# Performance work log

Measured on AMD Instinct MI355X. Metric: run time of the kernel, lower is better.

## Reference

```python
import jax, jax.numpy as jnp
import numpy as np

B, C, H, L = 8, 1, 512, 4096


def setup_inputs() -> dict:
    key = jax.random.key(0)
    k1, k2, k3, k4, k5 = jax.random.split(key, 5)
    u = jax.random.normal(k1, (B, H, L), dtype=jnp.float32)
    # SSM kernel k (C, H, L): stand-in for HippoSSKernel output, scaled so the
    # length-L convolution has O(1) variance.
    k = jax.random.normal(k2, (C, H, L), dtype=jnp.float32) * (1.0 / np.sqrt(L))
    D = jax.random.normal(k3, (C, H), dtype=jnp.float32)
    # output_linear: pointwise linear (C*H) -> H
    W = jax.random.normal(k4, (H, C * H), dtype=jnp.float32) * (1.0 / np.sqrt(C * H))
    b = jax.random.normal(k5, (H,), dtype=jnp.float32) * 0.01
    return {"u": u, "k": k, "D": D, "W": W, "b": b}


def reference(u, k, D, W, b):
    # u: (B, H, L), k: (C, H, L), D: (C, H), W: (H, C*H), b: (H,)
    Lq = u.shape[-1]
    n = 2 * Lq  # zero-padded FFT length for linear (non-circular) convolution
    k_f = jnp.fft.rfft(k, n=n)                       # (C, H, n//2+1) complex
    u_f = jnp.fft.rfft(u, n=n)                       # (B, H, n//2+1) complex
    y_f = jnp.einsum('bhl,chl->bchl', u_f, k_f)      # freq-domain multiply
    y = jnp.fft.irfft(y_f, n=n)[..., :Lq]            # (B, C, H, L)
    y = y + jnp.einsum('bhl,ch->bchl', u, D)         # skip term
    Bq, Cq, Hq, _ = y.shape
    y = y.reshape(Bq, Cq * Hq, Lq)                   # (B, C*H, L)
    y = jax.nn.gelu(y, approximate=False)            # torch GELU (erf)
    y = jnp.einsum('bcl,dc->bdl', y, W) + b[None, :, None]  # pointwise linear
    return y
```

## Files before the change

### kernel.cpp

```cpp
#include <hip/hip_runtime.h>
#include <hip/hip_bf16.h>
#include <math.h>

#define L_DIM 4096
#define H_DIM 512
#define B_DIM 8
#define SEG 2048

typedef __attribute__((ext_vector_type(8))) short short8;
typedef __attribute__((ext_vector_type(4))) float floatx4;

__device__ __forceinline__ unsigned f2bf(float f) {
    unsigned x = __float_as_uint(f);
    return (x + 0x7fffu + ((x >> 16) & 1u)) >> 16;
}

__global__ __launch_bounds__(256, 3) void conv_gelu_mfma(
    const float* __restrict__ u,
    const float* __restrict__ kk,
    const float* __restrict__ Dp,
    unsigned short* __restrict__ g,
    const float* __restrict__ W,
    unsigned short* __restrict__ Wb)
{
    __shared__ __align__(16) unsigned short kA[4144];
    __shared__ __align__(16) unsigned short kB[4144];
    __shared__ __align__(16) unsigned short us[8][2104];

    const int h   = blockIdx.x;
    const int Lb  = blockIdx.y << 10;
    const int tid = threadIdx.x;
    const int lane = tid & 63;
    const int w   = tid >> 6;
    const int i   = lane & 15;
    const int q   = lane >> 4;
    const int b   = i & 7;
    const int s   = i >> 3;

    if (Wb != nullptr && blockIdx.y == 0) {
        const float* wsrc = W + (size_t)h * H_DIM;
        unsigned short* wdst = Wb + (size_t)h * H_DIM;
        wdst[tid]       = (unsigned short)f2bf(wsrc[tid]);
        wdst[tid + 256] = (unsigned short)f2bf(wsrc[tid + 256]);
    }

    const float* kh = kk + (size_t)h * L_DIM;

    for (int p = tid; p < 4144; p += 256) {
        int t1 = L_DIM + 15 - p;
        int t2 = L_DIM + 14 - p;
        float v1 = (t1 >= 0 && t1 < L_DIM) ? kh[t1] : 0.0f;
        float v2 = (t2 >= 0 && t2 < L_DIM) ? kh[t2] : 0.0f;
        kA[p] = (unsigned short)f2bf(v1);
        kB[p] = (unsigned short)f2bf(v2);
    }

    floatx4 acc[8];
    #pragma unroll
    for (int t = 0; t < 8; t++) acc[t] = (floatx4){0.f, 0.f, 0.f, 0.f};

    const char* kbase = (const char*)((i & 1) ? kA : kB);
    const int aconst = 2 * (L_DIM + ((i & 1) ? 15 : 14) - i + 8 * q);
    const int basew = Lb + 32 * w;

    union AFrag { int x[4]; short8 v; };

    for (int seg = 0; seg < 2; seg++) {
        const int ms = seg * SEG;
        const int mstart = (seg == 0) ? -32 : SEG;
        const int segmax = ms + SEG - 32;
        if (seg == 1) {
            if (Lb + 992 < SEG) break;
            __syncthreads();
        }
        for (int e = tid * 4; e < 2096; e += 1024) {
            int m = ms - 32 + e;
            #pragma unroll
            for (int bb = 0; bb < 8; bb++) {
                float4 v = make_float4(0.f, 0.f, 0.f, 0.f);
                if (m >= 0 && m < L_DIM)
                    v = *(const float4*)(u + ((size_t)bb * H_DIM + h) * L_DIM + m);
                unsigned lo = f2bf(v.x) | (f2bf(v.y) << 16);
                unsigned hi = f2bf(v.z) | (f2bf(v.w) << 16);
                *(uint2*)&us[bb][e] = make_uint2(lo, hi);
            }
        }
        __syncthreads();

        const char* bbase = (const char*)&us[b][0] + 2 * (32 - ms + 16 * s + 8 * q);
        const char* ab = kbase + aconst;

        for (int c = 0; c < 4; c++) {
            const int c32 = 32 * c;
            const int rel = basew - c32;
            const int j_hi = (rel - mstart) >> 7;
            int j_lo = (rel - segmax + 127) >> 7;
            if (j_lo < -7) j_lo = -7;
            if (j_hi < j_lo) continue;
            const int n = j_hi - j_lo + 1;
            int n_pos = 0;
            if (j_hi >= 0) n_pos = j_hi - ((j_lo > 0) ? j_lo : 0) + 1;
            const int n_main = n_pos & ~7;

            const char* abase = ab - 2 * c32;
            const char* bb0 = bbase + 2 * (rel - 128 * j_hi);

            for (int jb = 0; jb < n_main; jb += 8) {
                const int j_g = j_hi - jb;
                const char* aptr = abase - 256 * (j_g + 7);
                const char* bptr = bb0 + 256 * jb;

                AFrag As[15];
                short8 Bs[8];
                Bs[0] = *(const short8*)(bptr);
                #pragma unroll
                for (int d = 7; d < 15; d++) {
                    const int* ap = (const int*)(aptr + 256 * (14 - d));
                    As[d].x[0] = ap[0]; As[d].x[1] = ap[1];
                    As[d].x[2] = ap[2]; As[d].x[3] = ap[3];
                }
                #pragma unroll
                for (int k = 1; k < 8; k++) {
                    Bs[k] = *(const short8*)(bptr + 256 * k);
                    const int* ap = (const int*)(aptr + 256 * (14 - (7 - k)));
                    As[7 - k].x[0] = ap[0]; As[7 - k].x[1] = ap[1];
                    As[7 - k].x[2] = ap[2]; As[7 - k].x[3] = ap[3];
                }
                __builtin_amdgcn_sched_barrier(0);

                #pragma unroll
                for (int k = 0; k < 8; k++)
                    #pragma unroll
                    for (int t = 0; t < 8; t++)
                        acc[t] = __builtin_amdgcn_mfma_f32_16x16x32_bf16(
                            As[7 - k + t].v, Bs[k], acc[t], 0, 0, 0);
            }

            if (n_main < n) {
                const int j_top = j_hi - n_main;
                AFrag Wd[8];
                #pragma unroll
                for (int d = 1; d < 8; d++) {
                    const int dd = c32 + (j_top + d) * 128;
                    if (dd >= 0) {
                        const int* ap = (const int*)(ab - 2 * dd);
                        Wd[d].x[0] = ap[0]; Wd[d].x[1] = ap[1];
                        Wd[d].x[2] = ap[2]; Wd[d].x[3] = ap[3];
                    } else {
                        Wd[d].x[0] = 0; Wd[d].x[1] = 0; Wd[d].x[2] = 0; Wd[d].x[3] = 0;
                    }
                }
                for (int jb = n_main; jb < n; jb += 8) {
                    #pragma unroll
                    for (int k = 0; k < 8; k++) {
                        const int jj = jb + k;
                        if (jj < n) {
                            const int dd0 = c32 + (j_hi - jj) * 128;
                            AFrag nf;
                            if (dd0 >= 0) {
                                const int* ap = (const int*)(ab - 2 * dd0);
                                nf.x[0] = ap[0]; nf.x[1] = ap[1];
                                nf.x[2] = ap[2]; nf.x[3] = ap[3];
                            } else {
                                nf.x[0] = 0; nf.x[1] = 0; nf.x[2] = 0; nf.x[3] = 0;
                            }
                            Wd[(8 - k) & 7] = nf;
                            short8 bf = *(const short8*)(bb0 + 256 * jj);
                            #pragma unroll
                            for (int t = 0; t < 8; t++)
                                acc[t] = __builtin_amdgcn_mfma_f32_16x16x32_bf16(
                                    Wd[(t - k) & 7].v, bf, acc[t], 0, 0, 0);
                        }
                    }
                }
            }
        }
    }

    const float Dh = Dp[h];
    #pragma unroll
    for (int t = 0; t < 8; t++) {
        const int l0 = Lb + 32 * w + 128 * t;
        const int lb2 = l0 + 16 * s + 4 * q;
        const size_t off = ((size_t)b * H_DIM + h) * L_DIM + lb2;
        float4 uv = *(const float4*)(u + off);
        float y0 = acc[t][0] + uv.x * Dh;
        float y1 = acc[t][1] + uv.y * Dh;
        float y2 = acc[t][2] + uv.z * Dh;
        float y3 = acc[t][3] + uv.w * Dh;
        const float c = 0.70710678118654752f;
        float g0 = 0.5f * y0 * (1.0f + erff(y0 * c));
        float g1 = 0.5f * y1 * (1.0f + erff(y1 * c));
        float g2 = 0.5f * y2 * (1.0f + erff(y2 * c));
        float g3 = 0.5f * y3 * (1.0f + erff(y3 * c));
        unsigned lo = f2bf(g0) | (f2bf(g1) << 16);
        unsigned hi = f2bf(g2) | (f2bf(g3) << 16);
        *(uint2*)(g + off) = make_uint2(lo, hi);
    }
}

template <bool PREW>
__global__ __launch_bounds__(256, 2) void pointwise_mfma(
    const unsigned short* __restrict__ g,
    const unsigned short* __restrict__ Wb,
    const float* __restrict__ W,
    const float* __restrict__ bias,
    float* __restrict__ out)
{
    __shared__ __align__(16) unsigned gs2[128 * 36];
    __shared__ __align__(16) unsigned short ws[256 * 76];

    const int tid = threadIdx.x;
    const int l0 = blockIdx.x * 128;
    const int d0 = blockIdx.y * 256;
    const int bz = blockIdx.z;
    const int w  = tid >> 6;
    const int lane = tid & 63;
    const int n  = lane & 15;
    const int q  = lane >> 4;

    const int p   = tid & 31;
    const int oct = tid >> 5;

    const int quarter = tid & 3;
    const int rb      = tid >> 2;

    floatx4 acc[8][4];
    #pragma unroll
    for (int mt = 0; mt < 8; mt++)
        #pragma unroll
        for (int nt = 0; nt < 4; nt++) acc[mt][nt] = (floatx4){0.f, 0.f, 0.f, 0.f};

    for (int c0 = 0; c0 < H_DIM; c0 += 64) {
        {
            const unsigned short* gp = g + ((size_t)bz * H_DIM + c0 + 2 * p) * L_DIM + l0 + 16 * oct;
            uint4 va0 = *(const uint4*)gp;
            uint4 va1 = *(const uint4*)(gp + 8);
            uint4 vb0 = *(const uint4*)(gp + L_DIM);
            uint4 vb1 = *(const uint4*)(gp + L_DIM + 8);
            #pragma unroll
            for (int half = 0; half < 2; half++) {
                const unsigned* ua = (const unsigned*)(half ? &va1 : &va0);
                const unsigned* ub = (const unsigned*)(half ? &vb1 : &vb0);
                #pragma unroll
                for (int e = 0; e < 4; e++) {
                    unsigned w0 = (ua[e] & 0xFFFFu) | (ub[e] << 16);
                    unsigned w1 = (ua[e] >> 16) | (ub[e] & 0xFFFF0000u);
                    const int lrow = 16 * oct + 8 * half + 2 * e;
                    gs2[lrow * 36 + p] = w0;
                    gs2[(lrow + 1) * 36 + p] = w1;
                }
            }
        }
        if (PREW) {
            #pragma unroll
            for (int gg = 0; gg < 4; gg++) {
                const int row = rb + 64 * gg;
                const unsigned short* wp = Wb + (size_t)(d0 + row) * H_DIM + c0 + 16 * quarter;
                uint4 w0 = ((const uint4*)wp)[0];
                uint4 w1 = ((const uint4*)wp)[1];
                *(uint4*)&ws[row * 76 + 16 * quarter]     = w0;
                *(uint4*)&ws[row * 76 + 16 * quarter + 8] = w1;
            }
        } else {
            #pragma unroll
            for (int gg = 0; gg < 4; gg++) {
                const int row = rb + 64 * gg;
                const float* wp = W + (size_t)(d0 + row) * H_DIM + c0 + 16 * quarter;
                float4 f0 = ((const float4*)wp)[0];
                float4 f1 = ((const float4*)wp)[1];
                float4 f2 = ((const float4*)wp)[2];
                float4 f3 = ((const float4*)wp)[3];
                unsigned o0 = f2bf(f0.x) | (f2bf(f0.y) << 16);
                unsigned o1 = f2bf(f0.z) | (f2bf(f0.w) << 16);
                unsigned o2 = f2bf(f1.x) | (f2bf(f1.y) << 16);
                unsigned o3 = f2bf(f1.z) | (f2bf(f1.w) << 16);
                unsigned o4 = f2bf(f2.x) | (f2bf(f2.y) << 16);
                unsigned o5 = f2bf(f2.z) | (f2bf(f2.w) << 16);
                unsigned o6 = f2bf(f3.x) | (f2bf(f3.y) << 16);
                unsigned o7 = f2bf(f3.z) | (f2bf(f3.w) << 16);
                *(uint4*)&ws[row * 76 + 16 * quarter]     = make_uint4(o0, o1, o2, o3);
                *(uint4*)&ws[row * 76 + 16 * quarter + 8] = make_uint4(o4, o5, o6, o7);
            }
        }
        __syncthreads();

        #pragma unroll
        for (int ks = 0; ks < 2; ks++) {
            short8 bfr[4];
            #pragma unroll
            for (int nt = 0; nt < 4; nt++)
                bfr[nt] = *(const short8*)&ws[(64 * w + 16 * nt + n) * 76 + 32 * ks + 8 * q];
            #pragma unroll
            for (int mt = 0; mt < 8; mt++) {
                union { uint4 u4; short8 v; } af;
                af.u4 = *(const uint4*)&gs2[(16 * mt + n) * 36 + 16 * ks + 4 * q];
                #pragma unroll
                for (int nt = 0; nt < 4; nt++)
                    acc[mt][nt] = __builtin_amdgcn_mfma_f32_16x16x32_bf16(af.v, bfr[nt], acc[mt][nt], 0, 0, 0);
            }
        }
        __syncthreads();
    }

    #pragma unroll
    for (int nt = 0; nt < 4; nt++) {
        const int d = d0 + 64 * w + 16 * nt + n;
        const float bb = bias[d];
        float* obase = out + ((size_t)bz * H_DIM + d) * L_DIM + l0 + 4 * q;
        #pragma unroll
        for (int mt = 0; mt < 8; mt++) {
            float4 r = make_float4(acc[mt][nt][0] + bb, acc[mt][nt][1] + bb,
                                   acc[mt][nt][2] + bb, acc[mt][nt][3] + bb);
            *(float4*)(obase + 16 * mt) = r;
        }
    }
}

extern "C" void kernel_launch(void* const* d_in, const int* in_sizes, int n_in,
                              void* d_out, int out_size, void* d_ws, size_t ws_size,
                              hipStream_t stream) {
    const float* u    = (const float*)d_in[0];
    const float* k    = (const float*)d_in[1];
    const float* D    = (const float*)d_in[2];
    const float* W    = (const float*)d_in[3];
    const float* bias = (const float*)d_in[4];
    float* out = (float*)d_out;
    unsigned short* g = (unsigned short*)d_ws;

    const size_t g_bytes = (size_t)B_DIM * H_DIM * L_DIM * sizeof(unsigned short);
    const size_t w_bytes = (size_t)H_DIM * H_DIM * sizeof(unsigned short);
    const bool prew = ws_size >= g_bytes + w_bytes;
    unsigned short* Wb = prew ? (unsigned short*)((char*)d_ws + g_bytes) : nullptr;

    conv_gelu_mfma<<<dim3(H_DIM, L_DIM / 1024), 256, 0, stream>>>(u, k, D, g, W, Wb);
    if (prew)
        pointwise_mfma<true><<<dim3(L_DIM / 128, H_DIM / 256, B_DIM), 256, 0, stream>>>(g, Wb, W, bias, out);
    else
        pointwise_mfma<false><<<dim3(L_DIM / 128, H_DIM / 256, B_DIM), 256, 0, stream>>>(g, nullptr, W, bias, out);
}
```

Before: 267.5 us.

## Widen conv blocks to 512 threads and software-pipeline pointwise GEMM loads

The conv+GELU kernel now uses 512-thread blocks, each covering 2048 output positions with 8 waves. This halves how often the kernel and u tiles are staged into shared memory per position. The specialised 8-step main MFMA loop with preloaded fragments is dropped in favour of the single sliding-window loop, which may cut instruction-level efficiency. The pointwise GEMM (PREW path) now prefetches the next tile's g and W into registers while computing the current one. That adds register pressure and an extra barrier per iteration.

Result: faster. 251.0 us (-6.2%).

```diff
diff --git a/kernel.cpp b/kernel.cpp
--- a/kernel.cpp
+++ b/kernel.cpp
@@ -15,7 +15,7 @@
     return (x + 0x7fffu + ((x >> 16) & 1u)) >> 16;
 }
 
-__global__ __launch_bounds__(256, 3) void conv_gelu_mfma(
+__global__ __launch_bounds__(512, 6) void conv_gelu_mfma(
     const float* __restrict__ u,
     const float* __restrict__ kk,
     const float* __restrict__ Dp,
@@ -28,7 +28,7 @@
     __shared__ __align__(16) unsigned short us[8][2104];
 
     const int h   = blockIdx.x;
-    const int Lb  = blockIdx.y << 10;
+    const int Lb  = blockIdx.y << 11;
     const int tid = threadIdx.x;
     const int lane = tid & 63;
     const int w   = tid >> 6;
@@ -40,13 +40,12 @@
     if (Wb != nullptr && blockIdx.y == 0) {
         const float* wsrc = W + (size_t)h * H_DIM;
         unsigned short* wdst = Wb + (size_t)h * H_DIM;
-        wdst[tid]       = (unsigned short)f2bf(wsrc[tid]);
-        wdst[tid + 256] = (unsigned short)f2bf(wsrc[tid + 256]);
+        wdst[tid] = (unsigned short)f2bf(wsrc[tid]);
     }
 
     const float* kh = kk + (size_t)h * L_DIM;
 
-    for (int p = tid; p < 4144; p += 256) {
+    for (int p = tid; p < 4144; p += 512) {
         int t1 = L_DIM + 15 - p;
         int t2 = L_DIM + 14 - p;
         float v1 = (t1 >= 0 && t1 < L_DIM) ? kh[t1] : 0.0f;
@@ -70,10 +69,10 @@
         const int mstart = (seg == 0) ? -32 : SEG;
         const int segmax = ms + SEG - 32;
         if (seg == 1) {
-            if (Lb + 992 < SEG) break;
+            if (Lb + 2016 < SEG) break;
             __syncthreads();
         }
-        for (int e = tid * 4; e < 2096; e += 1024) {
+        for (int e = tid * 4; e < 2096; e += 2048) {
             int m = ms - 32 + e;
             #pragma unroll
             for (int bb = 0; bb < 8; bb++) {
@@ -90,87 +89,51 @@
         const char* bbase = (const char*)&us[b][0] + 2 * (32 - ms + 16 * s + 8 * q);
         const char* ab = kbase + aconst;
 
-        for (int c = 0; c < 4; c++) {
+        for (int c = 0; c < 8; c++) {
             const int c32 = 32 * c;
             const int rel = basew - c32;
-            const int j_hi = (rel - mstart) >> 7;
-            int j_lo = (rel - segmax + 127) >> 7;
+            const int j_hi = (rel - mstart) >> 8;
+            int j_lo = (rel - segmax + 255) >> 8;
             if (j_lo < -7) j_lo = -7;
             if (j_hi < j_lo) continue;
             const int n = j_hi - j_lo + 1;
-            int n_pos = 0;
-            if (j_hi >= 0) n_pos = j_hi - ((j_lo > 0) ? j_lo : 0) + 1;
-            const int n_main = n_pos & ~7;
-
-            const char* abase = ab - 2 * c32;
-            const char* bb0 = bbase + 2 * (rel - 128 * j_hi);
-
-            for (int jb = 0; jb < n_main; jb += 8) {
-                const int j_g = j_hi - jb;
-                const char* aptr = abase - 256 * (j_g + 7);
-                const char* bptr = bb0 + 256 * jb;
-
-                AFrag As[15];
-                short8 Bs[8];
-                Bs[0] = *(const short8*)(bptr);
-                #pragma unroll
-                for (int d = 7; d < 15; d++) {
-                    const int* ap = (const int*)(aptr + 256 * (14 - d));
-                    As[d].x[0] = ap[0]; As[d].x[1] = ap[1];
-                    As[d].x[2] = ap[2]; As[d].x[3] = ap[3];
-                }
-                #pragma unroll
-                for (int k = 1; k < 8; k++) {
-                    Bs[k] = *(const short8*)(bptr + 256 * k);
-                    const int* ap = (const int*)(aptr + 256 * (14 - (7 - k)));
-                    As[7 - k].x[0] = ap[0]; As[7 - k].x[1] = ap[1];
-                    As[7 - k].x[2] = ap[2]; As[7 - k].x[3] = ap[3];
-                }
-                __builtin_amdgcn_sched_barrier(0);
-
-                #pragma unroll
-                for (int k = 0; k < 8; k++)
-                    #pragma unroll
-                    for (int t = 0; t < 8; t++)
-                        acc[t] = __builtin_amdgcn_mfma_f32_16x16x32_bf16(
-                            As[7 - k + t].v, Bs[k], acc[t], 0, 0, 0);
-            }
-
-            if (n_main < n) {
-                const int j_top = j_hi - n_main;
-                AFrag Wd[8];
-                #pragma unroll
-                for (int d = 1; d < 8; d++) {
-                    const int dd = c32 + (j_top + d) * 128;
-                    if (dd >= 0) {
-                        const int* ap = (const int*)(ab - 2 * dd);
-                        Wd[d].x[0] = ap[0]; Wd[d].x[1] = ap[1];
-                        Wd[d].x[2] = ap[2]; Wd[d].x[3] = ap[3];
-                    } else {
-                        Wd[d].x[0] = 0; Wd[d].x[1] = 0; Wd[d].x[2] = 0; Wd[d].x[3] = 0;
-                    }
-                }
-                for (int jb = n_main; jb < n; jb += 8) {
-                    #pragma unroll
-                    for (int k = 0; k < 8; k++) {
-                        const int jj = jb + k;
-                        if (jj < n) {
-                            const int dd0 = c32 + (j_hi - jj) * 128;
-                            AFrag nf;
-                            if (dd0 >= 0) {
-                                const int* ap = (const int*)(ab - 2 * dd0);
-                                nf.x[0] = ap[0]; nf.x[1] = ap[1];
-                                nf.x[2] = ap[2]; nf.x[3] = ap[3];
-                            } else {
-                                nf.x[0] = 0; nf.x[1] = 0; nf.x[2] = 0; nf.x[3] = 0;
-                            }
-                            Wd[(8 - k) & 7] = nf;
-                            short8 bf = *(const short8*)(bb0 + 256 * jj);
-                            #pragma unroll
-                            for (int t = 0; t < 8; t++)
-                                acc[t] = __builtin_amdgcn_mfma_f32_16x16x32_bf16(
-                                    Wd[(t - k) & 7].v, bf, acc[t], 0, 0, 0);
+
+            AFrag Wd[8];
+            #pragma unroll
+            for (int d = 1; d < 8; d++) {
+                const int dd = c32 + (j_hi + d) * 256;
+                if (dd >= 0) {
+                    const int* ap = (const int*)(ab - 2 * dd);
+                    Wd[d].x[0] = ap[0]; Wd[d].x[1] = ap[1];
+                    Wd[d].x[2] = ap[2]; Wd[d].x[3] = ap[3];
+                } else {
+                    Wd[d].x[0] = 0; Wd[d].x[1] = 0; Wd[d].x[2] = 0; Wd[d].x[3] = 0;
+                }
+            }
+
+            const char* aab = ab - 2 * c32 - 512 * j_hi;
+            const char* bb0 = bbase + 2 * (rel - 256 * j_hi);
+
+            for (int jb = 0; jb < n; jb += 8) {
+                #pragma unroll
+                for (int k = 0; k < 8; k++) {
+                    const int jj = jb + k;
+                    if (jj < n) {
+                        const int dd0 = c32 + (j_hi - jj) * 256;
+                        AFrag nf;
+                        if (dd0 >= 0) {
+                            const int* ap = (const int*)(aab + 512 * jj);
+                            nf.x[0] = ap[0]; nf.x[1] = ap[1];
+                            nf.x[2] = ap[2]; nf.x[3] = ap[3];
+                        } else {
+                            nf.x[0] = 0; nf.x[1] = 0; nf.x[2] = 0; nf.x[3] = 0;
                         }
+                        Wd[(8 - k) & 7] = nf;
+                        short8 bf = *(const short8*)(bb0 + 512 * jj);
+                        #pragma unroll
+                        for (int t = 0; t < 8; t++)
+                            acc[t] = __builtin_amdgcn_mfma_f32_16x16x32_bf16(
+                                Wd[(t - k) & 7].v, bf, acc[t], 0, 0, 0);
                     }
                 }
             }
@@ -180,7 +143,7 @@
     const float Dh = Dp[h];
     #pragma unroll
     for (int t = 0; t < 8; t++) {
-        const int l0 = Lb + 32 * w + 128 * t;
+        const int l0 = Lb + 32 * w + 256 * t;
         const int lb2 = l0 + 16 * s + 4 * q;
         const size_t off = ((size_t)b * H_DIM + h) * L_DIM + lb2;
         float4 uv = *(const float4*)(u + off);
@@ -231,76 +194,141 @@
         #pragma unroll
         for (int nt = 0; nt < 4; nt++) acc[mt][nt] = (floatx4){0.f, 0.f, 0.f, 0.f};
 
-    for (int c0 = 0; c0 < H_DIM; c0 += 64) {
-        {
-            const unsigned short* gp = g + ((size_t)bz * H_DIM + c0 + 2 * p) * L_DIM + l0 + 16 * oct;
-            uint4 va0 = *(const uint4*)gp;
-            uint4 va1 = *(const uint4*)(gp + 8);
-            uint4 vb0 = *(const uint4*)(gp + L_DIM);
-            uint4 vb1 = *(const uint4*)(gp + L_DIM + 8);
+    if (PREW) {
+        const unsigned short* gbase = g + ((size_t)bz * H_DIM + 2 * p) * L_DIM + l0 + 16 * oct;
+        const unsigned short* wbase = Wb + (size_t)(d0 + rb) * H_DIM + 16 * quarter;
+
+        uint4 ga0, ga1, gb0, gb1;
+        uint4 w00, w01, w10, w11, w20, w21, w30, w31;
+
+        auto loadT = [&](int c0) {
+            const unsigned short* gp = gbase + (size_t)c0 * L_DIM;
+            ga0 = *(const uint4*)gp;
+            ga1 = *(const uint4*)(gp + 8);
+            gb0 = *(const uint4*)(gp + L_DIM);
+            gb1 = *(const uint4*)(gp + L_DIM + 8);
+            const unsigned short* wp = wbase + c0;
+            w00 = ((const uint4*)wp)[0]; w01 = ((const uint4*)wp)[1]; wp += 64 * H_DIM;
+            w10 = ((const uint4*)wp)[0]; w11 = ((const uint4*)wp)[1]; wp += 64 * H_DIM;
+            w20 = ((const uint4*)wp)[0]; w21 = ((const uint4*)wp)[1]; wp += 64 * H_DIM;
+            w30 = ((const uint4*)wp)[0]; w31 = ((const uint4*)wp)[1];
+        };
+        auto writeT = [&]() {
             #pragma unroll
             for (int half = 0; half < 2; half++) {
-                const unsigned* ua = (const unsigned*)(half ? &va1 : &va0);
-                const unsigned* ub = (const unsigned*)(half ? &vb1 : &vb0);
+                const unsigned* ua = (const unsigned*)(half ? &ga1 : &ga0);
+                const unsigned* ub = (const unsigned*)(half ? &gb1 : &gb0);
                 #pragma unroll
                 for (int e = 0; e < 4; e++) {
-                    unsigned w0 = (ua[e] & 0xFFFFu) | (ub[e] << 16);
-                    unsigned w1 = (ua[e] >> 16) | (ub[e] & 0xFFFF0000u);
+                    unsigned lo16 = (ua[e] & 0xFFFFu) | (ub[e] << 16);
+                    unsigned hi16 = (ua[e] >> 16) | (ub[e] & 0xFFFF0000u);
                     const int lrow = 16 * oct + 8 * half + 2 * e;
-                    gs2[lrow * 36 + p] = w0;
-                    gs2[(lrow + 1) * 36 + p] = w1;
-                }
-            }
-        }
-        if (PREW) {
-            #pragma unroll
-            for (int gg = 0; gg < 4; gg++) {
-                const int row = rb + 64 * gg;
-                const unsigned short* wp = Wb + (size_t)(d0 + row) * H_DIM + c0 + 16 * quarter;
-                uint4 w0 = ((const uint4*)wp)[0];
-                uint4 w1 = ((const uint4*)wp)[1];
-                *(uint4*)&ws[row * 76 + 16 * quarter]     = w0;
-                *(uint4*)&ws[row * 76 + 16 * quarter + 8] = w1;
-            }
-        } else {
-            #pragma unroll
-            for (int gg = 0; gg < 4; gg++) {
-                const int row = rb + 64 * gg;
-                const float* wp = W + (size_t)(d0 + row) * H_DIM + c0 + 16 * quarter;
-                float4 f0 = ((const float4*)wp)[0];
-                float4 f1 = ((const float4*)wp)[1];
-                float4 f2 = ((const float4*)wp)[2];
-                float4 f3 = ((const float4*)wp)[3];
-                unsigned o0 = f2bf(f0.x) | (f2bf(f0.y) << 16);
-                unsigned o1 = f2bf(f0.z) | (f2bf(f0.w) << 16);
-                unsigned o2 = f2bf(f1.x) | (f2bf(f1.y) << 16);
-                unsigned o3 = f2bf(f1.z) | (f2bf(f1.w) << 16);
-                unsigned o4 = f2bf(f2.x) | (f2bf(f2.y) << 16);
-                unsigned o5 = f2bf(f2.z) | (f2bf(f2.w) << 16);
-                unsigned o6 = f2bf(f3.x) | (f2bf(f3.y) << 16);
-                unsigned o7 = f2bf(f3.z) | (f2bf(f3.w) << 16);
-                *(uint4*)&ws[row * 76 + 16 * quarter]     = make_uint4(o0, o1, o2, o3);
-                *(uint4*)&ws[row * 76 + 16 * quarter + 8] = make_uint4(o4, o5, o6, o7);
-            }
-        }
+                    gs2[lrow * 36 + p] = lo16;
+                    gs2[(lrow + 1) * 36 + p] = hi16;
+                }
+            }
+            *(uint4*)&ws[(rb      ) * 76 + 16 * quarter]     = w00;
+            *(uint4*)&ws[(rb      ) * 76 + 16 * quarter + 8] = w01;
+            *(uint4*)&ws[(rb +  64) * 76 + 16 * quarter]     = w10;
+            *(uint4*)&ws[(rb +  64) * 76 + 16 * quarter + 8] = w11;
+            *(uint4*)&ws[(rb + 128) * 76 + 16 * quarter]     = w20;
+            *(uint4*)&ws[(rb + 128) * 76 + 16 * quarter + 8] = w21;
+            *(uint4*)&ws[(rb + 192) * 76 + 16 * quarter]     = w30;
+            *(uint4*)&ws[(rb + 192) * 76 + 16 * quarter + 8] = w31;
+        };
+        auto computeT = [&]() {
+            #pragma unroll
+            for (int ks = 0; ks < 2; ks++) {
+                short8 bfr[4];
+                #pragma unroll
+                for (int nt = 0; nt < 4; nt++)
+                    bfr[nt] = *(const short8*)&ws[(64 * w + 16 * nt + n) * 76 + 32 * ks + 8 * q];
+                #pragma unroll
+                for (int mt = 0; mt < 8; mt++) {
+                    union { uint4 u4; short8 v; } af;
+                    af.u4 = *(const uint4*)&gs2[(16 * mt + n) * 36 + 16 * ks + 4 * q];
+                    #pragma unroll
+                    for (int nt = 0; nt < 4; nt++)
+                        acc[mt][nt] = __builtin_amdgcn_mfma_f32_16x16x32_bf16(af.v, bfr[nt], acc[mt][nt], 0, 0, 0);
+                }
+            }
+        };
+
+        loadT(0);
+        writeT();
         __syncthreads();
-
         #pragma unroll
-        for (int ks = 0; ks < 2; ks++) {
-            short8 bfr[4];
-            #pragma unroll
-            for (int nt = 0; nt < 4; nt++)
-                bfr[nt] = *(const short8*)&ws[(64 * w + 16 * nt + n) * 76 + 32 * ks + 8 * q];
-            #pragma unroll
-            for (int mt = 0; mt < 8; mt++) {
-                union { uint4 u4; short8 v; } af;
-                af.u4 = *(const uint4*)&gs2[(16 * mt + n) * 36 + 16 * ks + 4 * q];
+        for (int it = 0; it < 8; it++) {
+            if (it < 7) loadT(64 * (it + 1));
+            __builtin_amdgcn_sched_barrier(0);
+            computeT();
+            if (it < 7) {
+                __syncthreads();
+                writeT();
+                __syncthreads();
+            }
+        }
+    } else {
+        for (int c0 = 0; c0 < H_DIM; c0 += 64) {
+            {
+                const unsigned short* gp = g + ((size_t)bz * H_DIM + c0 + 2 * p) * L_DIM + l0 + 16 * oct;
+                uint4 va0 = *(const uint4*)gp;
+                uint4 va1 = *(const uint4*)(gp + 8);
+                uint4 vb0 = *(const uint4*)(gp + L_DIM);
+                uint4 vb1 = *(const uint4*)(gp + L_DIM + 8);
+                #pragma unroll
+                for (int half = 0; half < 2; half++) {
+                    const unsigned* ua = (const unsigned*)(half ? &va1 : &va0);
+                    const unsigned* ub = (const unsigned*)(half ? &vb1 : &vb0);
+                    #pragma unroll
+                    for (int e = 0; e < 4; e++) {
+                        unsigned w0 = (ua[e] & 0xFFFFu) | (ub[e] << 16);
+                        unsigned w1 = (ua[e] >> 16) | (ub[e] & 0xFFFF0000u);
+                        const int lrow = 16 * oct + 8 * half + 2 * e;
+                        gs2[lrow * 36 + p] = w0;
+                        gs2[(lrow + 1) * 36 + p] = w1;
+                    }
+                }
+            }
+            {
+                #pragma unroll
+                for (int gg = 0; gg < 4; gg++) {
+                    const int row = rb + 64 * gg;
+                    const float* wp = W + (size_t)(d0 + row) * H_DIM + c0 + 16 * quarter;
+                    float4 f0 = ((const float4*)wp)[0];
+                    float4 f1 = ((const float4*)wp)[1];
+                    float4 f2 = ((const float4*)wp)[2];
+                    float4 f3 = ((const float4*)wp)[3];
+                    unsigned o0 = f2bf(f0.x) | (f2bf(f0.y) << 16);
+                    unsigned o1 = f2bf(f0.z) | (f2bf(f0.w) << 16);
+                    unsigned o2 = f2bf(f1.x) | (f2bf(f1.y) << 16);
+                    unsigned o3 = f2bf(f1.z) | (f2bf(f1.w) << 16);
+                    unsigned o4 = f2bf(f2.x) | (f2bf(f2.y) << 16);
+                    unsigned o5 = f2bf(f2.z) | (f2bf(f2.w) << 16);
+                    unsigned o6 = f2bf(f3.x) | (f2bf(f3.y) << 16);
+                    unsigned o7 = f2bf(f3.z) | (f2bf(f3.w) << 16);
+                    *(uint4*)&ws[row * 76 + 16 * quarter]     = make_uint4(o0, o1, o2, o3);
+                    *(uint4*)&ws[row * 76 + 16 * quarter + 8] = make_uint4(o4, o5, o6, o7);
+                }
+            }
+            __syncthreads();
+            #pragma unroll
+            for (int ks = 0; ks < 2; ks++) {
+                short8 bfr[4];
                 #pragma unroll
                 for (int nt = 0; nt < 4; nt++)
-                    acc[mt][nt] = __builtin_amdgcn_mfma_f32_16x16x32_bf16(af.v, bfr[nt], acc[mt][nt], 0, 0, 0);
-            }
-        }
-        __syncthreads();
+                    bfr[nt] = *(const short8*)&ws[(64 * w + 16 * nt + n) * 76 + 32 * ks + 8 * q];
+                #pragma unroll
+                for (int mt = 0; mt < 8; mt++) {
+                    union { uint4 u4; short8 v; } af;
+                    af.u4 = *(const uint4*)&gs2[(16 * mt + n) * 36 + 16 * ks + 4 * q];
+                    #pragma unroll
+                    for (int nt = 0; nt < 4; nt++)
+                        acc[mt][nt] = __builtin_amdgcn_mfma_f32_16x16x32_bf16(af.v, bfr[nt], acc[mt][nt], 0, 0, 0);
+                }
+            }
+            __syncthreads();
+        }
     }
 
     #pragma unroll
@@ -333,7 +361,7 @@
     const bool prew = ws_size >= g_bytes + w_bytes;
     unsigned short* Wb = prew ? (unsigned short*)((char*)d_ws + g_bytes) : nullptr;
 
-    conv_gelu_mfma<<<dim3(H_DIM, L_DIM / 1024), 256, 0, stream>>>(u, k, D, g, W, Wb);
+    conv_gelu_mfma<<<dim3(H_DIM, L_DIM / 2048), 512, 0, stream>>>(u, k, D, g, W, Wb);
     if (prew)
         pointwise_mfma<true><<<dim3(L_DIM / 128, H_DIM / 256, B_DIM), 256, 0, stream>>>(g, Wb, W, bias, out);
     else
```
